# Kernel tuning notes

Measured on AMD Instinct MI355X. Metric: run time of the kernel, lower is better.

Reference implementation:

```python
import jax, jax.numpy as jnp
import numpy as np

D = 128
H = 4
L = 3
MAX_LEN = 696


def _pe(max_len, d):
    pos = jnp.arange(max_len, dtype=jnp.float32)[:, None]
    div = jnp.exp(jnp.arange(0, d, 2, dtype=jnp.float32) * (-jnp.log(jnp.float32(10000.0)) / d))
    pe = jnp.zeros((max_len, d), dtype=jnp.float32)
    pe = pe.at[:, 0::2].set(jnp.sin(pos * div))
    pe = pe.at[:, 1::2].set(jnp.cos(pos * div))
    return pe  # [max_len, d]


def _ln(x, w, b, eps=1e-5):
    m = jnp.mean(x, axis=-1, keepdims=True)
    v = jnp.mean((x - m) ** 2, axis=-1, keepdims=True)
    return (x - m) / jnp.sqrt(v + eps) * w + b


def _mha(xq, xkv, wqkv, bqkv, wo, bo, mask=None):
    # xq: [Tq,B,d], xkv: [Tk,B,d] (seq-first, torch convention)
    d = xq.shape[-1]
    hd = d // H
    q = xq @ wqkv[:d].T + bqkv[:d]
    k = xkv @ wqkv[d:2 * d].T + bqkv[d:2 * d]
    v = xkv @ wqkv[2 * d:].T + bqkv[2 * d:]

    def split(t):
        T, B, _ = t.shape
        return t.reshape(T, B, H, hd).transpose(1, 2, 0, 3)  # [B,H,T,hd]

    qh, kh, vh = split(q), split(k), split(v)
    s = jnp.einsum('bhqd,bhkd->bhqk', qh, kh) / jnp.sqrt(jnp.float32(hd))
    if mask is not None:
        s = jnp.where(mask, jnp.float32(-1e9), s)
    a = jax.nn.softmax(s, axis=-1)
    o = jnp.einsum('bhqk,bhkd->bhqd', a, vh)
    Tq, B = xq.shape[0], xq.shape[1]
    o = o.transpose(2, 0, 1, 3).reshape(Tq, B, d)
    return o @ wo.T + bo


def _forward(src, tgt, emb_in_w, emb_in_b, emb_out_w, emb_out_b,
             enc_qkv_w, enc_qkv_b, enc_proj_w, enc_proj_b,
             enc_ff1_w, enc_ff1_b, enc_ff2_w, enc_ff2_b, enc_ln_w, enc_ln_b,
             dec_sa_qkv_w, dec_sa_qkv_b, dec_sa_proj_w, dec_sa_proj_b,
             dec_ca_qkv_w, dec_ca_qkv_b, dec_ca_proj_w, dec_ca_proj_b,
             dec_ff1_w, dec_ff1_b, dec_ff2_w, dec_ff2_b, dec_ln_w, dec_ln_b,
             head_w, head_b):
    pe = _pe(MAX_LEN, D)
    # ---- encoder ----
    src_p = jnp.transpose(src, (2, 0, 1))  # [S,B,1]
    x = src_p @ emb_in_w.T + emb_in_b + pe[:src_p.shape[0], None, :]
    for i in range(L):
        a = _mha(x, x, enc_qkv_w[i], enc_qkv_b[i], enc_proj_w[i], enc_proj_b[i])
        x = _ln(x + a, enc_ln_w[i, 0], enc_ln_b[i, 0])
        f = jax.nn.relu(x @ enc_ff1_w[i].T + enc_ff1_b[i]) @ enc_ff2_w[i].T + enc_ff2_b[i]
        x = _ln(x + f, enc_ln_w[i, 1], enc_ln_b[i, 1])
    memory = x  # [S,B,D]
    # ---- decoder (full teacher forcing: loop collapses to one causal pass) ----
    tgt_p = jnp.transpose(tgt, (2, 0, 1))  # [T,B,1]
    T = tgt_p.shape[0]
    y = tgt_p[:T - 1] @ emb_out_w.T + emb_out_b  # [T-1,B,D]
    # original code applies pos encoding only to the initial token of the decode loop
    y = y.at[0].add(pe[0])
    mask = jnp.triu(jnp.ones((T - 1, T - 1), dtype=bool), k=1)  # True = masked
    for i in range(L):
        a = _mha(y, y, dec_sa_qkv_w[i], dec_sa_qkv_b[i], dec_sa_proj_w[i], dec_sa_proj_b[i], mask=mask)
        y = _ln(y + a, dec_ln_w[i, 0], dec_ln_b[i, 0])
        c = _mha(y, memory, dec_ca_qkv_w[i], dec_ca_qkv_b[i], dec_ca_proj_w[i], dec_ca_proj_b[i])
        y = _ln(y + c, dec_ln_w[i, 1], dec_ln_b[i, 1])
        f = jax.nn.relu(y @ dec_ff1_w[i].T + dec_ff1_b[i]) @ dec_ff2_w[i].T + dec_ff2_b[i]
        y = _ln(y + f, dec_ln_w[i, 2], dec_ln_b[i, 2])
    out = y @ head_w.T + head_b  # [T-1,B,1]
    return jnp.transpose(out, (1, 2, 0))  # [B,1,T-1]


def setup_inputs() -> dict:
    key = jax.random.key(0)
    ks = iter(jax.random.split(key, 64))

    def n(shape, s=0.02):
        return (jax.random.normal(next(ks), shape) * s).astype(jnp.float32)

    return {
        'src': jax.random.normal(next(ks), (64, 1, 696), dtype=jnp.float32),
        'tgt': jax.random.normal(next(ks), (64, 1, 512), dtype=jnp.float32),
        'emb_in_w': n((D, 1)), 'emb_in_b': n((D,)),
        'emb_out_w': n((D, 1)), 'emb_out_b': n((D,)),
        'enc_qkv_w': n((L, 3 * D, D)), 'enc_qkv_b': n((L, 3 * D)),
        'enc_proj_w': n((L, D, D)), 'enc_proj_b': n((L, D)),
        'enc_ff1_w': n((L, D, D)), 'enc_ff1_b': n((L, D)),
        'enc_ff2_w': n((L, D, D)), 'enc_ff2_b': n((L, D)),
        'enc_ln_w': jnp.ones((L, 2, D), dtype=jnp.float32),
        'enc_ln_b': jnp.zeros((L, 2, D), dtype=jnp.float32),
        'dec_sa_qkv_w': n((L, 3 * D, D)), 'dec_sa_qkv_b': n((L, 3 * D)),
        'dec_sa_proj_w': n((L, D, D)), 'dec_sa_proj_b': n((L, D)),
        'dec_ca_qkv_w': n((L, 3 * D, D)), 'dec_ca_qkv_b': n((L, 3 * D)),
        'dec_ca_proj_w': n((L, D, D)), 'dec_ca_proj_b': n((L, D)),
        'dec_ff1_w': n((L, D, D)), 'dec_ff1_b': n((L, D)),
        'dec_ff2_w': n((L, D, D)), 'dec_ff2_b': n((L, D)),
        'dec_ln_w': jnp.ones((L, 3, D), dtype=jnp.float32),
        'dec_ln_b': jnp.zeros((L, 3, D), dtype=jnp.float32),
        'head_w': n((1, D)), 'head_b': n((1,)),
    }


def reference(src, tgt, emb_in_w, emb_in_b, emb_out_w, emb_out_b,
              enc_qkv_w, enc_qkv_b, enc_proj_w, enc_proj_b,
              enc_ff1_w, enc_ff1_b, enc_ff2_w, enc_ff2_b, enc_ln_w, enc_ln_b,
              dec_sa_qkv_w, dec_sa_qkv_b, dec_sa_proj_w, dec_sa_proj_b,
              dec_ca_qkv_w, dec_ca_qkv_b, dec_ca_proj_w, dec_ca_proj_b,
              dec_ff1_w, dec_ff1_b, dec_ff2_w, dec_ff2_b, dec_ln_w, dec_ln_b,
              head_w, head_b):
    return _forward(src, tgt, emb_in_w, emb_in_b, emb_out_w, emb_out_b,
                    enc_qkv_w, enc_qkv_b, enc_proj_w, enc_proj_b,
                    enc_ff1_w, enc_ff1_b, enc_ff2_w, enc_ff2_b, enc_ln_w, enc_ln_b,
                    dec_sa_qkv_w, dec_sa_qkv_b, dec_sa_proj_w, dec_sa_proj_b,
                    dec_ca_qkv_w, dec_ca_qkv_b, dec_ca_proj_w, dec_ca_proj_b,
                    dec_ff1_w, dec_ff1_b, dec_ff2_w, dec_ff2_b, dec_ln_w, dec_ln_b,
                    head_w, head_b)
```

## Files before the change

### kernel.cpp

```cpp
#include <hip/hip_runtime.h>
#include <hip/hip_bf16.h>


typedef unsigned short u16;
typedef unsigned int u32;
typedef float f32x4 __attribute__((ext_vector_type(4)));
typedef float f32x2 __attribute__((ext_vector_type(2)));
typedef float f32x16 __attribute__((ext_vector_type(16)));
typedef unsigned short u16x8 __attribute__((ext_vector_type(8)));
typedef unsigned int u32x2 __attribute__((ext_vector_type(2)));
typedef unsigned int u32x4 __attribute__((ext_vector_type(4)));
typedef __bf16 bf16x8 __attribute__((ext_vector_type(8)));

static __device__ __forceinline__ float bf2f(u16 u) {
  u32 x = ((u32)u) << 16;
  return __builtin_bit_cast(float, x);
}
static __device__ __forceinline__ u16 f2bf(float f) {
  u32 x = __builtin_bit_cast(u32, f);
  u32 r = (x + 0x7fffu + ((x >> 16) & 1u)) >> 16;
  return (u16)r;
}
static __device__ __forceinline__ f32x4 mfma16(bf16x8 a, bf16x8 b, f32x4 c) {
  return __builtin_amdgcn_mfma_f32_16x16x32_bf16(a, b, c, 0, 0, 0);
}
static __device__ __forceinline__ f32x16 mfma32(bf16x8 a, bf16x8 b, f32x16 c) {
  return __builtin_amdgcn_mfma_f32_32x32x16_bf16(a, b, c, 0, 0, 0);
}
static __device__ __forceinline__ void plswap(u32& a, u32& b) {
  u32x2 r = __builtin_amdgcn_permlane32_swap(a, b, false, false);
  a = r.x; b = r.y;
}

__global__ void detect_k(const u32* __restrict__ ones, int* __restrict__ flag) {
  *flag = (ones[0] == 0x3F803F80u) ? 1 : 0;
}

struct CvtArgs {
  const void* p[32];
  int n[32];
  int off[32];
};

__global__ __launch_bounds__(256) void cvt_all(CvtArgs A, const int* __restrict__ flag,
                                               float* __restrict__ poolf,
                                               u16* __restrict__ poolb) {
  int ti = blockIdx.y;
  int i = blockIdx.x * 256 + threadIdx.x;
  int n = A.n[ti];
  if (i >= n) return;
  int o = A.off[ti] + i;
  if (*flag) {
    u16 raw = ((const u16*)A.p[ti])[i];
    poolb[o] = raw;
    poolf[o] = bf2f(raw);
  } else {
    float v = ((const float*)A.p[ti])[i];
    poolf[o] = v;
    poolb[o] = f2bf(v);
  }
}

__global__ void embed_enc(const float* __restrict__ src, const float* __restrict__ w,
                          const float* __restrict__ b, float* __restrict__ X,
                          u16* __restrict__ Xb) {
  int s = blockIdx.x, d = threadIdx.x;
  float freq = __expf(-(float)(d & 126) * 0.07195578415606394f);
  float arg = (float)s * freq;
  float pe = (d & 1) ? cosf(arg) : sinf(arg);
  float wd = w[d], bd = b[d];
  for (int bb = 0; bb < 64; ++bb) {
    float v = src[bb * 696 + s] * wd + bd + pe;
    size_t o = ((size_t)s * 64 + bb) * 128 + d;
    X[o] = v;
    Xb[o] = f2bf(v);
  }
}

__global__ void embed_dec(const float* __restrict__ tgt, const float* __restrict__ w,
                          const float* __restrict__ b, float* __restrict__ Y,
                          u16* __restrict__ Yb) {
  int tt = blockIdx.x, d = threadIdx.x;
  float wd = w[d], bd = b[d];
  float pe0 = (tt == 0 && (d & 1)) ? 1.0f : 0.0f;
  for (int bb = 0; bb < 64; ++bb) {
    float v = tgt[bb * 512 + tt] * wd + bd + pe0;
    size_t o = ((size_t)tt * 64 + bb) * 128 + d;
    Y[o] = v;
    Yb[o] = f2bf(v);
  }
}

__global__ __launch_bounds__(256) void gemm_ln(
    const u16* __restrict__ Xb, const u16* __restrict__ Wb,
    const float* __restrict__ bias, float* __restrict__ R,
    u16* __restrict__ Rb, const float* __restrict__ lnw,
    const float* __restrict__ lnb) {
  __shared__ u16 Ws[128][136];
  const int t = threadIdx.x;
  const int n0 = blockIdx.x << 6;
  const int wv = t >> 6, lane = t & 63, lg = lane >> 4, lr = lane & 15;
  const int r0 = n0 + (wv << 4);

#pragma unroll
  for (int i = 0; i < 8; ++i) {
    int idx = t + (i << 8);
    int r = idx >> 4, c = (idx & 15) << 3;
    *(u16x8*)&Ws[r][c] = *(const u16x8*)(Wb + ((size_t)r << 7) + c);
  }
  bf16x8 afr[4];
  const int arow = r0 + lr;
#pragma unroll
  for (int ks = 0; ks < 4; ++ks)
    afr[ks] = *(const bf16x8*)(Xb + ((size_t)arow << 7) + (ks << 5) + (lg << 3));
  __syncthreads();

  f32x4 acc[8] = {};
#pragma unroll
  for (int ks = 0; ks < 4; ++ks) {
#pragma unroll
    for (int cb = 0; cb < 8; ++cb) {
      bf16x8 bfr = *(const bf16x8*)&Ws[(cb << 4) + lr][(ks << 5) + (lg << 3)];
      acc[cb] = mfma16(afr[ks], bfr, acc[cb]);
    }
  }

  float vals[8][4];
#pragma unroll
  for (int cb = 0; cb < 8; ++cb) {
    float bv = bias[(cb << 4) + lr];
#pragma unroll
    for (int r = 0; r < 4; ++r) {
      size_t row = (size_t)(r0 + (lg << 2) + r);
      vals[cb][r] = acc[cb][r] + bv + R[(row << 7) + (cb << 4) + lr];
    }
  }
  float mean[4], rstd[4];
#pragma unroll
  for (int r = 0; r < 4; ++r) {
    float s = 0.0f, s2 = 0.0f;
#pragma unroll
    for (int cb = 0; cb < 8; ++cb) {
      float v = vals[cb][r];
      s += v; s2 += v * v;
    }
    s += __shfl_xor(s, 1); s2 += __shfl_xor(s2, 1);
    s += __shfl_xor(s, 2); s2 += __shfl_xor(s2, 2);
    s += __shfl_xor(s, 4); s2 += __shfl_xor(s2, 4);
    s += __shfl_xor(s, 8); s2 += __shfl_xor(s2, 8);
    float m = s * 0.0078125f;
    float var = s2 * 0.0078125f - m * m;
    mean[r] = m;
    rstd[r] = rsqrtf(var + 1e-5f);
  }
#pragma unroll
  for (int cb = 0; cb < 8; ++cb) {
    float w = lnw[(cb << 4) + lr], bb = lnb[(cb << 4) + lr];
#pragma unroll
    for (int r = 0; r < 4; ++r) {
      float v = (vals[cb][r] - mean[r]) * rstd[r] * w + bb;
      size_t o = ((size_t)(r0 + (lg << 2) + r) << 7) + (cb << 4) + lr;
      R[o] = v;
      Rb[o] = f2bf(v);
    }
  }
}

__global__ __launch_bounds__(256) void gemm_plff(
    const u16* __restrict__ Ab, const u16* __restrict__ Wp, const float* __restrict__ bp,
    const u16* __restrict__ W1, const float* __restrict__ b1,
    const u16* __restrict__ W2, const float* __restrict__ b2,
    float* __restrict__ R, u16* __restrict__ Rb,
    const float* __restrict__ ln1w, const float* __restrict__ ln1b,
    const float* __restrict__ ln2w, const float* __restrict__ ln2b) {
  __shared__ u16 WBUF[128][136];
  __shared__ u16 XBUF[64][136];
  const int t = threadIdx.x;
  const int n0 = blockIdx.x << 6;
  const int wv = t >> 6, lane = t & 63, lg = lane >> 4, lr = lane & 15;
  const int r0 = n0 + (wv << 4);

#pragma unroll
  for (int i = 0; i < 8; ++i) {
    int idx = t + (i << 8);
    int r = idx >> 4, c = (idx & 15) << 3;
    *(u16x8*)&WBUF[r][c] = *(const u16x8*)(Wp + ((size_t)r << 7) + c);
  }
  bf16x8 afr[4];
#pragma unroll
  for (int ks = 0; ks < 4; ++ks)
    afr[ks] = *(const bf16x8*)(Ab + ((size_t)(r0 + lr) << 7) + (ks << 5) + (lg << 3));
  __syncthreads();

  f32x4 acc[8] = {};
#pragma unroll
  for (int ks = 0; ks < 4; ++ks) {
#pragma unroll
    for (int cb = 0; cb < 8; ++cb) {
      bf16x8 bfr = *(const bf16x8*)&WBUF[(cb << 4) + lr][(ks << 5) + (lg << 3)];
      acc[cb] = mfma16(afr[ks], bfr, acc[cb]);
    }
  }
  float x1[8][4];
#pragma unroll
  for (int cb = 0; cb < 8; ++cb) {
    float bv = bp[(cb << 4) + lr];
#pragma unroll
    for (int r = 0; r < 4; ++r) {
      size_t row = (size_t)(r0 + (lg << 2) + r);
      x1[cb][r] = acc[cb][r] + bv + R[(row << 7) + (cb << 4) + lr];
    }
  }
#pragma unroll
  for (int r = 0; r < 4; ++r) {
    float s = 0.0f, s2 = 0.0f;
#pragma unroll
    for (int cb = 0; cb < 8; ++cb) { float v = x1[cb][r]; s += v; s2 += v * v; }
    s += __shfl_xor(s, 1); s2 += __shfl_xor(s2, 1);
    s += __shfl_xor(s, 2); s2 += __shfl_xor(s2, 2);
    s += __shfl_xor(s, 4); s2 += __shfl_xor(s2, 4);
    s += __shfl_xor(s, 8); s2 += __shfl_xor(s2, 8);
    float m = s * 0.0078125f;
    float rstd = rsqrtf(s2 * 0.0078125f - m * m + 1e-5f);
#pragma unroll
    for (int cb = 0; cb < 8; ++cb)
      x1[cb][r] = (x1[cb][r] - m) * rstd * ln1w[(cb << 4) + lr] + ln1b[(cb << 4) + lr];
  }
#pragma unroll
  for (int cb = 0; cb < 8; ++cb)
#pragma unroll
    for (int r = 0; r < 4; ++r)
      XBUF[(wv << 4) + (lg << 2) + r][(cb << 4) + lr] = f2bf(x1[cb][r]);
  __syncthreads();

#pragma unroll
  for (int i = 0; i < 8; ++i) {
    int idx = t + (i << 8);
    int r = idx >> 4, c = (idx & 15) << 3;
    *(u16x8*)&WBUF[r][c] = *(const u16x8*)(W1 + ((size_t)r << 7) + c);
  }
#pragma unroll
  for (int ks = 0; ks < 4; ++ks)
    afr[ks] = *(const bf16x8*)&XBUF[(wv << 4) + lr][(ks << 5) + (lg << 3)];
  __syncthreads();

#pragma unroll
  for (int cb = 0; cb < 8; ++cb) acc[cb] = f32x4{0, 0, 0, 0};
#pragma unroll
  for (int ks = 0; ks < 4; ++ks) {
#pragma unroll
    for (int cb = 0; cb < 8; ++cb) {
      bf16x8 bfr = *(const bf16x8*)&WBUF[(cb << 4) + lr][(ks << 5) + (lg << 3)];
      acc[cb] = mfma16(afr[ks], bfr, acc[cb]);
    }
  }
  float h[8][4];
#pragma unroll
  for (int cb = 0; cb < 8; ++cb) {
    float bv = b1[(cb << 4) + lr];
#pragma unroll
    for (int r = 0; r < 4; ++r) h[cb][r] = fmaxf(acc[cb][r] + bv, 0.0f);
  }
  __syncthreads();

#pragma unroll
  for (int cb = 0; cb < 8; ++cb)
#pragma unroll
    for (int r = 0; r < 4; ++r)
      XBUF[(wv << 4) + (lg << 2) + r][(cb << 4) + lr] = f2bf(h[cb][r]);
#pragma unroll
  for (int i = 0; i < 8; ++i) {
    int idx = t + (i << 8);
    int r = idx >> 4, c = (idx & 15) << 3;
    *(u16x8*)&WBUF[r][c] = *(const u16x8*)(W2 + ((size_t)r << 7) + c);
  }
  __syncthreads();

#pragma unroll
  for (int ks = 0; ks < 4; ++ks)
    afr[ks] = *(const bf16x8*)&XBUF[(wv << 4) + lr][(ks << 5) + (lg << 3)];
#pragma unroll
  for (int cb = 0; cb < 8; ++cb) acc[cb] = f32x4{0, 0, 0, 0};
#pragma unroll
  for (int ks = 0; ks < 4; ++ks) {
#pragma unroll
    for (int cb = 0; cb < 8; ++cb) {
      bf16x8 bfr = *(const bf16x8*)&WBUF[(cb << 4) + lr][(ks << 5) + (lg << 3)];
      acc[cb] = mfma16(afr[ks], bfr, acc[cb]);
    }
  }
  float vals[8][4];
#pragma unroll
  for (int cb = 0; cb < 8; ++cb) {
    float bv = b2[(cb << 4) + lr];
#pragma unroll
    for (int r = 0; r < 4; ++r) vals[cb][r] = acc[cb][r] + bv + x1[cb][r];
  }
#pragma unroll
  for (int r = 0; r < 4; ++r) {
    float s = 0.0f, s2 = 0.0f;
#pragma unroll
    for (int cb = 0; cb < 8; ++cb) { float v = vals[cb][r]; s += v; s2 += v * v; }
    s += __shfl_xor(s, 1); s2 += __shfl_xor(s2, 1);
    s += __shfl_xor(s, 2); s2 += __shfl_xor(s2, 2);
    s += __shfl_xor(s, 4); s2 += __shfl_xor(s2, 4);
    s += __shfl_xor(s, 8); s2 += __shfl_xor(s2, 8);
    float m = s * 0.0078125f;
    float rstd = rsqrtf(s2 * 0.0078125f - m * m + 1e-5f);
#pragma unroll
    for (int cb = 0; cb < 8; ++cb) {
      float v = (vals[cb][r] - m) * rstd * ln2w[(cb << 4) + lr] + ln2b[(cb << 4) + lr];
      size_t o = ((size_t)(r0 + (lg << 2) + r) << 7) + (cb << 4) + lr;
      R[o] = v;
      Rb[o] = f2bf(v);
    }
  }
}

__global__ __launch_bounds__(256) void gemm_qkv(
    const u16* __restrict__ Xb, const u16* __restrict__ Wb,
    const float* __restrict__ bias, u16* __restrict__ Qg,
    u16* __restrict__ Kg, u16* __restrict__ Vg, int M, int kbase, int vbase) {
  __shared__ u16 Xs[64][136];
  __shared__ u16 Ws[64][136];
  const int t = threadIdx.x;
  const int n0 = blockIdx.x << 6, m0 = blockIdx.y << 6;
  const int wq = t >> 6, lane = t & 63, lg = lane >> 4, lr = lane & 15;
  const int wr = (wq >> 1) << 5, wc = (wq & 1) << 5;
  const float QS = 0.17677669529663687f * 1.4426950408889634f;

#pragma unroll
  for (int i = 0; i < 4; ++i) {
    int idx = t + (i << 8);
    int r = idx >> 4, c = (idx & 15) << 3;
    *(u16x8*)&Xs[r][c] = *(const u16x8*)(Xb + (size_t)(n0 + r) * 128 + c);
    *(u16x8*)&Ws[r][c] = *(const u16x8*)(Wb + (size_t)(m0 + r) * 128 + c);
  }
  __syncthreads();

  f32x4 acc00 = {0,0,0,0}, acc01 = {0,0,0,0}, acc10 = {0,0,0,0}, acc11 = {0,0,0,0};
#pragma unroll
  for (int ks = 0; ks < 4; ++ks) {
    bf16x8 a0 = *(const bf16x8*)&Xs[wr + lr][(ks << 5) + (lg << 3)];
    bf16x8 a1 = *(const bf16x8*)&Xs[wr + 16 + lr][(ks << 5) + (lg << 3)];
    bf16x8 b0 = *(const bf16x8*)&Ws[wc + lr][(ks << 5) + (lg << 3)];
    bf16x8 b1 = *(const bf16x8*)&Ws[wc + 16 + lr][(ks << 5) + (lg << 3)];
    acc00 = mfma16(a0, b0, acc00);
    acc01 = mfma16(a0, b1, acc01);
    acc10 = mfma16(a1, b0, acc10);
    acc11 = mfma16(a1, b1, acc11);
  }

  f32x4 accs[2][2] = {{acc00, acc01}, {acc10, acc11}};
#pragma unroll
  for (int mi = 0; mi < 2; ++mi) {
#pragma unroll
    for (int ni = 0; ni < 2; ++ni) {
      int col = m0 + wc + (ni << 4) + lr;
      float bv = bias[col];
#pragma unroll
      for (int r = 0; r < 4; ++r) {
        int row = n0 + wr + (mi << 4) + (lg << 2) + r;
        float v = accs[mi][ni][r] + bv;
        size_t ro = (size_t)row << 7;
        if (col < kbase) {
          Qg[ro + col] = f2bf(v * QS);
        } else if (col < vbase) {
          Kg[ro + (col - kbase)] = f2bf(v);
        } else {
          Vg[ro + (col - vbase)] = f2bf(v);
        }
      }
    }
  }
}

__global__ __launch_bounds__(256) void attn_g(
    const u16* __restrict__ Qg, const u16* __restrict__ Kg,
    const u16* __restrict__ Vg, u16* __restrict__ Ob,
    int Tq, int Tk, int causal, int bpb) {
  __shared__ u16 Ks[64][44];
  __shared__ u16 Vs[32][74];
  __shared__ float Lw[4][36];
  const int t = threadIdx.x;
  const int wv = t >> 6, lane = t & 63;
  const int lq = lane & 31, hi = lane >> 5;
  const int p = blockIdx.x;
  const int idx = p >> 3;
  const int bh = ((p & 7) << 5) + idx / bpb;
  const int blk = idx % bpb;
  const int nstrips = (Tq + 31) >> 5;
  const int strip = blk * 4 + wv;
  const bool active = strip < nstrips;
  const int b = bh >> 2, h = bh & 3;
  const int qw = (active ? strip : (nstrips - 1)) << 5;

  bf16x8 qf[2];
  {
    int ql = qw + lq; if (ql > Tq - 1) ql = Tq - 1;
    const u16* qp = Qg + (((size_t)ql * 64 + b) << 7) + h * 32 + (hi << 3);
    qf[0] = *(const bf16x8*)qp;
    qf[1] = *(const bf16x8*)(qp + 16);
  }

  f32x16 o = {};
  float lsum = 0.0f;

  const int nfull = causal ? (qw >> 6) : (Tk >> 6);
  int lastcol = causal ? qw + 31 : Tk - 1;
  if (lastcol > Tk - 1) lastcol = Tk - 1;
  int ntiles = (lastcol >> 6) + 1;
  if (!active) ntiles = 0;

  int lastq_blk = blk * 128 + 127;
  if (lastq_blk > Tq - 1) lastq_blk = Tq - 1;
  int lastcol_blk = causal ? lastq_blk : Tk - 1;
  if (lastcol_blk > Tk - 1) lastcol_blk = Tk - 1;
  const int ntb = (lastcol_blk >> 6) + 1;

  const int stok = t >> 2, sc = (t & 3) << 3;

  for (int kt = 0; kt < ntb; ++kt) {
    const int k0 = kt << 6;
    __syncthreads();
    {
      int tok = k0 + stok; if (tok > Tk - 1) tok = Tk - 1;
      size_t roff = (((size_t)tok * 64 + b) << 7) + h * 32 + sc;
      *(u16x8*)&Ks[stok][sc] = *(const u16x8*)(Kg + roff);
      u16x8 vv = *(const u16x8*)(Vg + roff);
#pragma unroll
      for (int e = 0; e < 8; ++e) Vs[sc + e][stok] = vv[e];
    }
    __syncthreads();
    if (kt >= ntiles) continue;
    const bool masked = (kt >= nfull);

#pragma unroll
    for (int kb = 0; kb < 2; ++kb) {
      const int krow = (kb << 5) + lq;
      bf16x8 ka0 = *(const bf16x8*)&Ks[krow][hi << 3];
      bf16x8 ka1 = *(const bf16x8*)&Ks[krow][16 + (hi << 3)];
      f32x16 s = {};
      __builtin_amdgcn_s_setprio(1);
      s = mfma32(ka0, qf[0], s);
      s = mfma32(ka1, qf[1], s);
      __builtin_amdgcn_s_setprio(0);

      float pv[16];
#pragma unroll
      for (int r = 0; r < 16; ++r) {
        float sv = s[r];
        if (masked) {
          int kk = k0 + (kb << 5) + (r & 3) + ((r >> 2) << 3) + (hi << 2);
          int q = qw + lq;
          bool ok = causal ? (kk <= q) : (kk < Tk);
          sv = ok ? sv : -1e30f;
        }
        float e = exp2f(sv);
        pv[r] = e;
        lsum += e;
      }
      u32 u[8];
#pragma unroll
      for (int m = 0; m < 8; ++m)
        asm("v_cvt_pk_bf16_f32 %0, %1, %2" : "=v"(u[m]) : "v"(pv[2 * m]), "v"(pv[2 * m + 1]));

#pragma unroll
      for (int c = 0; c < 2; ++c) {
        u32 a0 = u[4 * c + 0], b0 = u[4 * c + 2];
        u32 a1 = u[4 * c + 1], b1 = u[4 * c + 3];
        plswap(a0, b0);
        plswap(a1, b1);
        u32x4 wv4 = {a0, a1, b0, b1};
        bf16x8 pf = __builtin_bit_cast(bf16x8, wv4);
        bf16x8 vf = *(const bf16x8*)&Vs[lq][(kb << 5) + (c << 4) + (hi << 3)];
        __builtin_amdgcn_s_setprio(1);
        o = mfma32(pf, vf, o);
        __builtin_amdgcn_s_setprio(0);
      }
    }
  }

  if (active) {
    float lt = lsum + __shfl_xor(lsum, 32);
    if (hi == 0) Lw[wv][lq] = 1.0f / lt;
    f32x4 li[4];
#pragma unroll
    for (int g = 0; g < 4; ++g)
      li[g] = *(const f32x4*)&Lw[wv][(hi << 2) + (g << 3)];
#pragma unroll
    for (int r = 0; r < 16; ++r) {
      int q = qw + (r & 3) + ((r >> 2) << 3) + (hi << 2);
      if (q < Tq) {
        Ob[(((size_t)q * 64 + b) << 7) + h * 32 + lq] = f2bf(o[r] * li[r >> 2][r & 3]);
      }
    }
  }
}

__global__ __launch_bounds__(256) void head_k(
    const float* __restrict__ Y, const float* __restrict__ w,
    const float* __restrict__ bh, void* __restrict__ out, const int* __restrict__ flag) {
  int n = (blockIdx.x << 2) + (threadIdx.x >> 6);
  int lane = threadIdx.x & 63;
  const float* yp = Y + (size_t)n * 128 + (lane << 1);
  float s = yp[0] * w[lane << 1] + yp[1] * w[(lane << 1) + 1];
#pragma unroll
  for (int off = 1; off < 64; off <<= 1) s += __shfl_xor(s, off);
  if (lane == 0) {
    int tt = n >> 6, bb = n & 63;
    float r = s + bh[0];
    int idx = bb * 511 + tt;
    if (*flag) ((u16*)out)[idx] = f2bf(r);
    else       ((float*)out)[idx] = r;
  }
}

extern "C" void kernel_launch(void* const* d_in, const int* in_sizes, int n_in,
                              void* d_out, int out_size, void* d_ws, size_t ws_size,
                              hipStream_t stream) {
  (void)out_size; (void)ws_size;
  CvtArgs A;
  long off[33]; off[0] = 0;
  int maxn = 0;
  for (int i = 0; i < 32; ++i) {
    int n = (i < n_in) ? in_sizes[i] : 0;
    A.p[i] = (i < n_in) ? d_in[i] : d_in[0];
    A.n[i] = n;
    A.off[i] = (int)off[i];
    off[i + 1] = off[i] + n;
    if (n > maxn) maxn = n;
  }
  const size_t offA = (size_t)((off[32] + 15) & ~15l);

  const size_t NE = 44544;
  const size_t ND = 32704;
  float* ws   = (float*)d_ws;
  int*   flag = (int*)d_ws;
  float* Wp   = ws + 16;
  float* Xe   = Wp + offA;
  float* Yd   = Xe + NE * 128;
  u16*   U    = (u16*)(Yd + ND * 128);
  u16*   Wb   = U;
  u16*   Xebf = Wb + offA;
  u16*   Ydbf = Xebf + NE * 128;
  u16*   TMPbf= Ydbf + ND * 128;
  u16*   Qgb  = TMPbf + NE * 128;
  u16*   Kgb  = Qgb + NE * 128;
  u16*   Vgb  = Kgb + NE * 128;

  const float* F = Wp;
  detect_k<<<1, 1, 0, stream>>>((const u32*)d_in[14], flag);
  cvt_all<<<dim3((maxn + 255) / 256, 32), 256, 0, stream>>>(A, flag, Wp, Wb);

  embed_enc<<<dim3(696), dim3(128), 0, stream>>>(F + A.off[0], F + A.off[2], F + A.off[3], Xe, Xebf);
  for (int i = 0; i < 3; ++i) {
    gemm_qkv<<<dim3(696, 6), 256, 0, stream>>>(Xebf, Wb + A.off[6] + i * 49152, F + A.off[7] + i * 384,
                                               Qgb, Kgb, Vgb, 384, 128, 256);
    attn_g<<<dim3(1536), 256, 0, stream>>>(Qgb, Kgb, Vgb, TMPbf, 696, 696, 0, 6);
    gemm_plff<<<dim3(696), 256, 0, stream>>>(TMPbf, Wb + A.off[8] + i * 16384, F + A.off[9] + i * 128,
                                             Wb + A.off[10] + i * 16384, F + A.off[11] + i * 128,
                                             Wb + A.off[12] + i * 16384, F + A.off[13] + i * 128,
                                             Xe, Xebf,
                                             F + A.off[14] + (i * 2 + 0) * 128, F + A.off[15] + (i * 2 + 0) * 128,
                                             F + A.off[14] + (i * 2 + 1) * 128, F + A.off[15] + (i * 2 + 1) * 128);
  }

  embed_dec<<<dim3(511), dim3(128), 0, stream>>>(F + A.off[1], F + A.off[4], F + A.off[5], Yd, Ydbf);
  for (int i = 0; i < 3; ++i) {
    gemm_qkv<<<dim3(511, 6), 256, 0, stream>>>(Ydbf, Wb + A.off[16] + i * 49152, F + A.off[17] + i * 384,
                                               Qgb, Kgb, Vgb, 384, 128, 256);
    attn_g<<<dim3(1024), 256, 0, stream>>>(Qgb, Kgb, Vgb, TMPbf, 511, 511, 1, 4);
    gemm_ln<<<dim3(511), 256, 0, stream>>>(TMPbf, Wb + A.off[18] + i * 16384, F + A.off[19] + i * 128,
                                           Yd, Ydbf, F + A.off[28] + (i * 3 + 0) * 128, F + A.off[29] + (i * 3 + 0) * 128);
    gemm_qkv<<<dim3(511, 2), 256, 0, stream>>>(Ydbf, Wb + A.off[20] + i * 49152, F + A.off[21] + i * 384,
                                               Qgb, nullptr, nullptr, 128, 128, 128);
    gemm_qkv<<<dim3(696, 4), 256, 0, stream>>>(Xebf, Wb + A.off[20] + i * 49152 + 16384, F + A.off[21] + i * 384 + 128,
                                               nullptr, Kgb, Vgb, 256, 0, 128);
    attn_g<<<dim3(1024), 256, 0, stream>>>(Qgb, Kgb, Vgb, TMPbf, 511, 696, 0, 4);
    gemm_plff<<<dim3(511), 256, 0, stream>>>(TMPbf, Wb + A.off[22] + i * 16384, F + A.off[23] + i * 128,
                                             Wb + A.off[24] + i * 16384, F + A.off[25] + i * 128,
                                             Wb + A.off[26] + i * 16384, F + A.off[27] + i * 128,
                                             Yd, Ydbf,
                                             F + A.off[28] + (i * 3 + 1) * 128, F + A.off[29] + (i * 3 + 1) * 128,
                                             F + A.off[28] + (i * 3 + 2) * 128, F + A.off[29] + (i * 3 + 2) * 128);
  }

  head_k<<<dim3(8176), 256, 0, stream>>>(Yd, F + A.off[30], F + A.off[31], d_out, flag);
}
```

Measured before the change: 761.7 us.

## Fuse decoder self-attn LN with cross-attn Q projection; compute softmax denominators via MFMA

The decoder's self-attention projection+LayerNorm kernel now also runs the cross-attention Q projection from LDS-staged normalized rows. This removes one launch and the bf16 round trip of Ydbf, whose write is dropped, which assumes no later kernel reads it. Separately, attention computes the row sums of exp scores with an extra MFMA against a ones vector, replacing scalar accumulation, shuffles and an LDS exchange. That adds MFMA work per tile and sums the bf16-rounded probabilities.

Result: slower. 795.7 us (+4.5%).

```diff
diff --git a/kernel.cpp b/kernel.cpp
--- a/kernel.cpp
+++ b/kernel.cpp
@@ -91,28 +91,28 @@
   }
 }
 
-__global__ __launch_bounds__(256) void gemm_ln(
-    const u16* __restrict__ Xb, const u16* __restrict__ Wb,
-    const float* __restrict__ bias, float* __restrict__ R,
-    u16* __restrict__ Rb, const float* __restrict__ lnw,
-    const float* __restrict__ lnb) {
-  __shared__ u16 Ws[128][136];
+__global__ __launch_bounds__(256) void gemm_lnq(
+    const u16* __restrict__ Ab, const u16* __restrict__ Wp, const float* __restrict__ bp,
+    float* __restrict__ R, const float* __restrict__ ln1w, const float* __restrict__ ln1b,
+    const u16* __restrict__ Wq, const float* __restrict__ bq, u16* __restrict__ Qg) {
+  __shared__ u16 WBUF[128][136];
+  __shared__ u16 XBUF[64][136];
   const int t = threadIdx.x;
   const int n0 = blockIdx.x << 6;
   const int wv = t >> 6, lane = t & 63, lg = lane >> 4, lr = lane & 15;
   const int r0 = n0 + (wv << 4);
+  const float QS = 0.17677669529663687f * 1.4426950408889634f;
 
 #pragma unroll
   for (int i = 0; i < 8; ++i) {
     int idx = t + (i << 8);
     int r = idx >> 4, c = (idx & 15) << 3;
-    *(u16x8*)&Ws[r][c] = *(const u16x8*)(Wb + ((size_t)r << 7) + c);
+    *(u16x8*)&WBUF[r][c] = *(const u16x8*)(Wp + ((size_t)r << 7) + c);
   }
   bf16x8 afr[4];
-  const int arow = r0 + lr;
 #pragma unroll
   for (int ks = 0; ks < 4; ++ks)
-    afr[ks] = *(const bf16x8*)(Xb + ((size_t)arow << 7) + (ks << 5) + (lg << 3));
+    afr[ks] = *(const bf16x8*)(Ab + ((size_t)(r0 + lr) << 7) + (ks << 5) + (lg << 3));
   __syncthreads();
 
   f32x4 acc[8] = {};
@@ -120,48 +120,73 @@
   for (int ks = 0; ks < 4; ++ks) {
 #pragma unroll
     for (int cb = 0; cb < 8; ++cb) {
-      bf16x8 bfr = *(const bf16x8*)&Ws[(cb << 4) + lr][(ks << 5) + (lg << 3)];
+      bf16x8 bfr = *(const bf16x8*)&WBUF[(cb << 4) + lr][(ks << 5) + (lg << 3)];
       acc[cb] = mfma16(afr[ks], bfr, acc[cb]);
     }
   }
-
-  float vals[8][4];
+  float x1[8][4];
 #pragma unroll
   for (int cb = 0; cb < 8; ++cb) {
-    float bv = bias[(cb << 4) + lr];
+    float bv = bp[(cb << 4) + lr];
 #pragma unroll
     for (int r = 0; r < 4; ++r) {
       size_t row = (size_t)(r0 + (lg << 2) + r);
-      vals[cb][r] = acc[cb][r] + bv + R[(row << 7) + (cb << 4) + lr];
-    }
-  }
-  float mean[4], rstd[4];
+      x1[cb][r] = acc[cb][r] + bv + R[(row << 7) + (cb << 4) + lr];
+    }
+  }
 #pragma unroll
   for (int r = 0; r < 4; ++r) {
     float s = 0.0f, s2 = 0.0f;
 #pragma unroll
-    for (int cb = 0; cb < 8; ++cb) {
-      float v = vals[cb][r];
-      s += v; s2 += v * v;
-    }
+    for (int cb = 0; cb < 8; ++cb) { float v = x1[cb][r]; s += v; s2 += v * v; }
     s += __shfl_xor(s, 1); s2 += __shfl_xor(s2, 1);
     s += __shfl_xor(s, 2); s2 += __shfl_xor(s2, 2);
     s += __shfl_xor(s, 4); s2 += __shfl_xor(s2, 4);
     s += __shfl_xor(s, 8); s2 += __shfl_xor(s2, 8);
     float m = s * 0.0078125f;
-    float var = s2 * 0.0078125f - m * m;
-    mean[r] = m;
-    rstd[r] = rsqrtf(var + 1e-5f);
+    float rstd = rsqrtf(s2 * 0.0078125f - m * m + 1e-5f);
+#pragma unroll
+    for (int cb = 0; cb < 8; ++cb)
+      x1[cb][r] = (x1[cb][r] - m) * rstd * ln1w[(cb << 4) + lr] + ln1b[(cb << 4) + lr];
+  }
+#pragma unroll
+  for (int cb = 0; cb < 8; ++cb)
+#pragma unroll
+    for (int r = 0; r < 4; ++r) {
+      size_t o = ((size_t)(r0 + (lg << 2) + r) << 7) + (cb << 4) + lr;
+      R[o] = x1[cb][r];
+      XBUF[(wv << 4) + (lg << 2) + r][(cb << 4) + lr] = f2bf(x1[cb][r]);
+    }
+  __syncthreads();
+
+#pragma unroll
+  for (int i = 0; i < 8; ++i) {
+    int idx = t + (i << 8);
+    int r = idx >> 4, c = (idx & 15) << 3;
+    *(u16x8*)&WBUF[r][c] = *(const u16x8*)(Wq + ((size_t)r << 7) + c);
+  }
+#pragma unroll
+  for (int ks = 0; ks < 4; ++ks)
+    afr[ks] = *(const bf16x8*)&XBUF[(wv << 4) + lr][(ks << 5) + (lg << 3)];
+  __syncthreads();
+
+#pragma unroll
+  for (int cb = 0; cb < 8; ++cb) acc[cb] = f32x4{0, 0, 0, 0};
+#pragma unroll
+  for (int ks = 0; ks < 4; ++ks) {
+#pragma unroll
+    for (int cb = 0; cb < 8; ++cb) {
+      bf16x8 bfr = *(const bf16x8*)&WBUF[(cb << 4) + lr][(ks << 5) + (lg << 3)];
+      acc[cb] = mfma16(afr[ks], bfr, acc[cb]);
+    }
   }
 #pragma unroll
   for (int cb = 0; cb < 8; ++cb) {
-    float w = lnw[(cb << 4) + lr], bb = lnb[(cb << 4) + lr];
+    float bv = bq[(cb << 4) + lr];
 #pragma unroll
     for (int r = 0; r < 4; ++r) {
-      float v = (vals[cb][r] - mean[r]) * rstd[r] * w + bb;
       size_t o = ((size_t)(r0 + (lg << 2) + r) << 7) + (cb << 4) + lr;
-      R[o] = v;
-      Rb[o] = f2bf(v);
+      Qg[o] = f2bf((acc[cb][r] + bv) * QS);
     }
   }
 }
@@ -381,7 +406,6 @@
     int Tq, int Tk, int causal, int bpb) {
   __shared__ u16 Ks[64][44];
   __shared__ u16 Vs[32][74];
-  __shared__ float Lw[4][36];
   const int t = threadIdx.x;
   const int wv = t >> 6, lane = t & 63;
   const int lq = lane & 31, hi = lane >> 5;
@@ -402,9 +426,10 @@
     qf[0] = *(const bf16x8*)qp;
     qf[1] = *(const bf16x8*)(qp + 16);
   }
-
-  f32x16 o = {};
-  float lsum = 0.0f;
+  const u32x4 onev = {0x3F803F80u, 0x3F803F80u, 0x3F803F80u, 0x3F803F80u};
+  const bf16x8 ones8 = __builtin_bit_cast(bf16x8, onev);
+
+  f32x16 o = {}, ol = {};
 
   const int nfull = causal ? (qw >> 6) : (Tk >> 6);
   int lastcol = causal ? qw + 31 : Tk - 1;
@@ -456,9 +481,7 @@
           bool ok = causal ? (kk <= q) : (kk < Tk);
           sv = ok ? sv : -1e30f;
         }
-        float e = exp2f(sv);
-        pv[r] = e;
-        lsum += e;
+        pv[r] = exp2f(sv);
       }
       u32 u[8];
 #pragma unroll
@@ -476,23 +499,18 @@
         bf16x8 vf = *(const bf16x8*)&Vs[lq][(kb << 5) + (c << 4) + (hi << 3)];
         __builtin_amdgcn_s_setprio(1);
         o = mfma32(pf, vf, o);
+        ol = mfma32(pf, ones8, ol);
         __builtin_amdgcn_s_setprio(0);
       }
     }
   }
 
   if (active) {
-    float lt = lsum + __shfl_xor(lsum, 32);
-    if (hi == 0) Lw[wv][lq] = 1.0f / lt;
-    f32x4 li[4];
-#pragma unroll
-    for (int g = 0; g < 4; ++g)
-      li[g] = *(const f32x4*)&Lw[wv][(hi << 2) + (g << 3)];
 #pragma unroll
     for (int r = 0; r < 16; ++r) {
       int q = qw + (r & 3) + ((r >> 2) << 3) + (hi << 2);
       if (q < Tq) {
-        Ob[(((size_t)q * 64 + b) << 7) + h * 32 + lq] = f2bf(o[r] * li[r >> 2][r & 3]);
+        Ob[(((size_t)q * 64 + b) << 7) + h * 32 + lq] = f2bf(o[r] / ol[r]);
       }
     }
   }
@@ -571,10 +589,9 @@
     gemm_qkv<<<dim3(511, 6), 256, 0, stream>>>(Ydbf, Wb + A.off[16] + i * 49152, F + A.off[17] + i * 384,
                                                Qgb, Kgb, Vgb, 384, 128, 256);
     attn_g<<<dim3(1024), 256, 0, stream>>>(Qgb, Kgb, Vgb, TMPbf, 511, 511, 1, 4);
-    gemm_ln<<<dim3(511), 256, 0, stream>>>(TMPbf, Wb + A.off[18] + i * 16384, F + A.off[19] + i * 128,
-                                           Yd, Ydbf, F + A.off[28] + (i * 3 + 0) * 128, F + A.off[29] + (i * 3 + 0) * 128);
-    gemm_qkv<<<dim3(511, 2), 256, 0, stream>>>(Ydbf, Wb + A.off[20] + i * 49152, F + A.off[21] + i * 384,
-                                               Qgb, nullptr, nullptr, 128, 128, 128);
+    gemm_lnq<<<dim3(511), 256, 0, stream>>>(TMPbf, Wb + A.off[18] + i * 16384, F + A.off[19] + i * 128,
+                                            Yd, F + A.off[28] + (i * 3 + 0) * 128, F + A.off[29] + (i * 3 + 0) * 128,
+                                            Wb + A.off[20] + i * 49152, F + A.off[21] + i * 384, Qgb);
     gemm_qkv<<<dim3(696, 4), 256, 0, stream>>>(Xebf, Wb + A.off[20] + i * 49152 + 16384, F + A.off[21] + i * 384 + 128,
                                                nullptr, Kgb, Vgb, 256, 0, 128);
     attn_g<<<dim3(1024), 256, 0, stream>>>(Qgb, Kgb, Vgb, TMPbf, 511, 696, 0, 4);
```
